# Optimization experiments

Measured on AMD Instinct MI355X. Metric: run time of the kernel, lower is better.

Reference implementation:

```python
import jax, jax.numpy as jnp
import numpy as np

G, T, D_IN, D_OUT = 8, 4096, 1024, 4096


def setup_inputs() -> dict:
    key = jax.random.key(0)
    k1, k2, k3 = jax.random.split(key, 3)
    x = jax.random.normal(k1, (T, D_IN), dtype=jnp.float32)
    # cumulative end offsets per group: sorted, last == T (grouped_mm convention)
    cuts = jnp.sort(jax.random.randint(k2, (G - 1,), 0, T, dtype=jnp.int32))
    offs = jnp.concatenate([cuts, jnp.array([T], dtype=jnp.int32)])
    weight = jax.random.normal(k3, (G, D_OUT, D_IN), dtype=jnp.float32) * (D_IN ** -0.5)
    return {"input": x, "grouped_mm_offs": offs, "weight": weight}


def reference(input, grouped_mm_offs, weight):
    # Grouped GEMM: row t (with offs[g-1] <= t < offs[g]) -> input[t] @ weight[g].T
    n_tok = input.shape[0]
    tok = jnp.arange(n_tok)
    gid = jnp.searchsorted(grouped_mm_offs, tok, side="right")  # [T] group id per row
    # Dense all-expert projection [G, T, D_OUT], then select the routed expert per row.
    proj = jnp.einsum("ti,goi->gto", input, weight)
    return proj[gid, tok]  # [T, D_OUT]
```

## Files before the change

kernel.cpp:

```cpp
#include <hip/hip_runtime.h>
#include <hip/hip_bf16.h>

#define NG 8
#define NT 4096
#define DIN 1024
#define DOUT 4096
#define BM 128
#define BN 128
#define BK 32
#define KTILES (DIN / BK)

typedef __attribute__((ext_vector_type(4))) float f32x4;
typedef __attribute__((ext_vector_type(8))) short bf16x8;

__device__ __forceinline__ void gld16(const float* g, float* l) {
    __builtin_amdgcn_global_load_lds(
        (const __attribute__((address_space(1))) void*)(g),
        (__attribute__((address_space(3))) void*)(l), 16, 0, 0);
}

__device__ __forceinline__ bf16x8 cvt8(f32x4 lo, f32x4 hi) {
    union { bf16x8 v; unsigned short s[8]; } u;
    union { __hip_bfloat16 h; unsigned short b; } t;
    t.h = __float2bfloat16(lo[0]); u.s[0] = t.b;
    t.h = __float2bfloat16(lo[1]); u.s[1] = t.b;
    t.h = __float2bfloat16(lo[2]); u.s[2] = t.b;
    t.h = __float2bfloat16(lo[3]); u.s[3] = t.b;
    t.h = __float2bfloat16(hi[0]); u.s[4] = t.b;
    t.h = __float2bfloat16(hi[1]); u.s[5] = t.b;
    t.h = __float2bfloat16(hi[2]); u.s[6] = t.b;
    t.h = __float2bfloat16(hi[3]); u.s[7] = t.b;
    return u.v;
}

__global__ __launch_bounds__(256, 2)
void grouped_gemm_bf16(const float* __restrict__ x,
                       const int* __restrict__ offs,
                       const float* __restrict__ w,
                       float* __restrict__ out) {
    __shared__ float lds[2 * 2 * BM * BK];

    const int rt = blockIdx.y;
    const int n0 = blockIdx.x * BN;
    int row0 = 0, endg = 0, gsel = -1;
    {
        int acc = 0, prev = 0;
        for (int g = 0; g < NG; ++g) {
            int e = offs[g];
            int cnt = (e - prev + BM - 1) / BM;
            if (rt < acc + cnt) { gsel = g; row0 = prev + (rt - acc) * BM; endg = e; break; }
            acc += cnt; prev = e;
        }
    }
    if (gsel < 0) return;
    const float* wg = w + (size_t)gsel * DOUT * DIN;

    const int tid  = threadIdx.x;
    const int lane = tid & 63;
    const int wid  = tid >> 6;
    const int wr   = wid >> 1, wc = wid & 1;
    const int lrow = lane & 15, kgrp = lane >> 4;

    int aoff[4], boff[4], sbase[4];
    #pragma unroll
    for (int i = 0; i < 4; ++i) {
        int stripe = i * 4 + wid;
        int r = stripe * 8 + (lane >> 3);
        int cs = (lane & 7) ^ (r & 7);
        int ar = row0 + r; if (ar >= endg) ar = endg - 1;
        aoff[i]  = ar * DIN + cs * 4;
        boff[i]  = (n0 + r) * DIN + cs * 4;
        sbase[i] = stripe * 256;
    }

    f32x4 acc[4][4];
    #pragma unroll
    for (int m = 0; m < 4; ++m)
        #pragma unroll
        for (int n = 0; n < 4; ++n)
            acc[m][n] = (f32x4){0.f, 0.f, 0.f, 0.f};

    {
        float* bA = lds;
        float* bB = lds + BM * BK;
        #pragma unroll
        for (int i = 0; i < 4; ++i) {
            gld16(x  + aoff[i], bA + sbase[i]);
            gld16(wg + boff[i], bB + sbase[i]);
        }
    }
    __syncthreads();

    for (int kt = 0; kt < KTILES; ++kt) {
        const int cur = kt & 1;

        if (kt + 1 < KTILES) {
            const int k0 = (kt + 1) * BK;
            float* bA = lds + (cur ^ 1) * (2 * BM * BK);
            float* bB = bA + BM * BK;
            #pragma unroll
            for (int i = 0; i < 4; ++i) {
                gld16(x  + aoff[i] + k0, bA + sbase[i]);
                gld16(wg + boff[i] + k0, bB + sbase[i]);
            }
        }

        {
            const float* bA = lds + cur * (2 * BM * BK);
            const float* bB = bA + BM * BK;
            bf16x8 af[4], bb[4];
            #pragma unroll
            for (int m = 0; m < 4; ++m) {
                int tr = wr * 64 + m * 16 + lrow;
                const float* p = bA + tr * BK;
                int c0 = (kgrp * 2)     ^ (tr & 7);
                int c1 = (kgrp * 2 + 1) ^ (tr & 7);
                af[m] = cvt8(*(const f32x4*)(p + c0 * 4), *(const f32x4*)(p + c1 * 4));
            }
            #pragma unroll
            for (int n = 0; n < 4; ++n) {
                int tr = wc * 64 + n * 16 + lrow;
                const float* p = bB + tr * BK;
                int c0 = (kgrp * 2)     ^ (tr & 7);
                int c1 = (kgrp * 2 + 1) ^ (tr & 7);
                bb[n] = cvt8(*(const f32x4*)(p + c0 * 4), *(const f32x4*)(p + c1 * 4));
            }
            #pragma unroll
            for (int m = 0; m < 4; ++m)
                #pragma unroll
                for (int n = 0; n < 4; ++n)
                    acc[m][n] = __builtin_amdgcn_mfma_f32_16x16x32_bf16(
                        af[m], bb[n], acc[m][n], 0, 0, 0);
        }

        __syncthreads();
    }

    #pragma unroll
    for (int m = 0; m < 4; ++m) {
        #pragma unroll
        for (int j = 0; j < 4; ++j) {
            int row = row0 + wr * 64 + m * 16 + (lane >> 4) * 4 + j;
            if (row < endg) {
                #pragma unroll
                for (int n = 0; n < 4; ++n) {
                    int col = n0 + wc * 64 + n * 16 + lrow;
                    out[(size_t)row * DOUT + col] = acc[m][n][j];
                }
            }
        }
    }
}

extern "C" void kernel_launch(void* const* d_in, const int* in_sizes, int n_in,
                              void* d_out, int out_size, void* d_ws, size_t ws_size,
                              hipStream_t stream) {
    const float* x    = (const float*)d_in[0];
    const int*   offs = (const int*)d_in[1];
    const float* w    = (const float*)d_in[2];
    float* out = (float*)d_out;

    dim3 grid(DOUT / BN, NT / BM + NG, 1);
    grouped_gemm_bf16<<<grid, 256, 0, stream>>>(x, offs, w, out);
}
```

Baseline: 85.88 us.

## Triple-buffer LDS tiles with vmcnt-based waits and single barrier per k-step

Replaces the double-buffered LDS pipeline with a three-stage ring that prefetches two k-tiles ahead. Each iteration waits for the older tile's loads with s_waitcnt vmcnt instead of draining everything, and uses one raw barrier per step in place of two __syncthreads. This is meant to hide more global-load latency, but LDS grows to 96KB and launch bounds drop to one block per CU, reducing occupancy.

```diff
diff --git a/kernel.cpp b/kernel.cpp
--- a/kernel.cpp
+++ b/kernel.cpp
@@ -33,12 +33,12 @@
     return u.v;
 }
 
-__global__ __launch_bounds__(256, 2)
+__global__ __launch_bounds__(256, 1)
 void grouped_gemm_bf16(const float* __restrict__ x,
                        const int* __restrict__ offs,
                        const float* __restrict__ w,
                        float* __restrict__ out) {
-    __shared__ float lds[2 * 2 * BM * BK];
+    __shared__ float lds[3 * 2 * BM * BK];
 
     const int rt = blockIdx.y;
     const int n0 = blockIdx.x * BN;
@@ -80,33 +80,34 @@
         for (int n = 0; n < 4; ++n)
             acc[m][n] = (f32x4){0.f, 0.f, 0.f, 0.f};
 
-    {
-        float* bA = lds;
-        float* bB = lds + BM * BK;
+    auto STAGE = [&](int kt, int buf) {
+        const int k0 = kt * BK;
+        float* bA = lds + buf * (2 * BM * BK);
+        float* bB = bA + BM * BK;
         #pragma unroll
         for (int i = 0; i < 4; ++i) {
-            gld16(x  + aoff[i], bA + sbase[i]);
-            gld16(wg + boff[i], bB + sbase[i]);
+            gld16(x  + aoff[i] + k0, bA + sbase[i]);
+            gld16(wg + boff[i] + k0, bB + sbase[i]);
         }
-    }
-    __syncthreads();
+    };
+
+    STAGE(0, 0);
+    STAGE(1, 1);
 
     for (int kt = 0; kt < KTILES; ++kt) {
-        const int cur = kt & 1;
+        if (kt < KTILES - 1) {
+            asm volatile("s_waitcnt vmcnt(8)" ::: "memory");
+        } else {
+            asm volatile("s_waitcnt vmcnt(0)" ::: "memory");
+        }
+        __builtin_amdgcn_s_barrier();
+        __builtin_amdgcn_sched_barrier(0);
 
-        if (kt + 1 < KTILES) {
-            const int k0 = (kt + 1) * BK;
-            float* bA = lds + (cur ^ 1) * (2 * BM * BK);
-            float* bB = bA + BM * BK;
-            #pragma unroll
-            for (int i = 0; i < 4; ++i) {
-                gld16(x  + aoff[i] + k0, bA + sbase[i]);
-                gld16(wg + boff[i] + k0, bB + sbase[i]);
-            }
-        }
+        if (kt + 2 < KTILES) STAGE(kt + 2, (kt + 2) % 3);
+        __builtin_amdgcn_sched_barrier(0);
 
         {
-            const float* bA = lds + cur * (2 * BM * BK);
+            const float* bA = lds + (kt % 3) * (2 * BM * BK);
             const float* bB = bA + BM * BK;
             bf16x8 af[4], bb[4];
             #pragma unroll
@@ -132,15 +133,13 @@
                     acc[m][n] = __builtin_amdgcn_mfma_f32_16x16x32_bf16(
                         af[m], bb[n], acc[m][n], 0, 0, 0);
         }
-
-        __syncthreads();
     }
 
     #pragma unroll
     for (int m = 0; m < 4; ++m) {
         #pragma unroll
         for (int j = 0; j < 4; ++j) {
-            int row = row0 + wr * 64 + m * 16 + (lane >> 4) * 4 + j;
+            int row = row0 + wr * 64 + m * 16 + kgrp * 4 + j;
             if (row < endg) {
                 #pragma unroll
                 for (int n = 0; n < 4; ++n) {
```

Result: slower. 138.0 us (+60.6%).
